# Performance work log

Measured on AMD Instinct MI355X. Metric: run time of the kernel, lower is better.

The kernel has to match this reference:

```python
import jax, jax.numpy as jnp
import numpy as np
from jax import lax

DN = ('NCHW', 'OIHW', 'NCHW')
EPS = 1e-5


def _conv3x3(x, w, b):
    return lax.conv_general_dilated(x, w, (1, 1), 'SAME', dimension_numbers=DN) + b[:, None, None]


def _conv1x1(x, w, b):
    return jnp.einsum('bchw,oc->bohw', x, w) + b[:, None, None]


def _dwconv3x3(x, w, b):
    # w: (C,1,3,3), depthwise
    C = x.shape[1]
    return lax.conv_general_dilated(x, w, (1, 1), 'SAME', feature_group_count=C,
                                    dimension_numbers=DN) + b[:, None, None]


def setup_inputs() -> dict:
    key = jax.random.key(0)
    ks = jax.random.split(key, 24)
    b, t, c, h, w = 2, 8, 64, 160, 160
    r, K = c // 4, 3

    def n(k, shape, s=0.05):
        return jax.random.normal(k, shape, dtype=jnp.float32) * s

    return {
        'feature': n(ks[0], (b, t, c, h, w), 1.0),
        'kc_w1': n(ks[1], (r, c)),
        'kc_bn_gamma': jnp.ones((r,), jnp.float32),
        'kc_bn_beta': jnp.zeros((r,), jnp.float32),
        'kc_bn_mean': jnp.zeros((r,), jnp.float32),
        'kc_bn_var': jnp.ones((r,), jnp.float32),
        'kc_w2': n(ks[2], (c * K * K, r)),
        'kc_b2': n(ks[3], (c * K * K,)),
        'kc_bias': n(ks[4], (c,)),
        'conv1_w': n(ks[5], (2 * c, 2 * c, 3, 3)),
        'conv1_b': n(ks[6], (2 * c,)),
        'pi1_w': n(ks[7], (4 * c, c)),
        'pi1_b': n(ks[8], (4 * c,)),
        'dw1_w': n(ks[9], (4 * c, 1, 3, 3)),
        'dw1_b': n(ks[10], (4 * c,)),
        'po1_w': n(ks[11], (c, 4 * c)),
        'po1_b': n(ks[12], (c,)),
        'pi2_w': n(ks[13], (4 * c, c)),
        'pi2_b': n(ks[14], (4 * c,)),
        'dw2_w': n(ks[15], (4 * c, 1, 3, 3)),
        'dw2_b': n(ks[16], (4 * c,)),
        'po2_w': n(ks[17], (c, 4 * c)),
        'po2_b': n(ks[18], (c,)),
    }


def reference(feature, kc_w1, kc_bn_gamma, kc_bn_beta, kc_bn_mean, kc_bn_var,
              kc_w2, kc_b2, kc_bias, conv1_w, conv1_b,
              pi1_w, pi1_b, dw1_w, dw1_b, po1_w, po1_b,
              pi2_w, pi2_b, dw2_w, dw2_b, po2_w, po2_b):
    b, t, c, h, w = feature.shape
    K = int(round((kc_w2.shape[0] // c) ** 0.5))  # dynamic kernel size (3)

    def dyn_dwconv(x_feat, y):
        # kernel generation: GAP -> 1x1 -> BN(eval) -> ReLU -> 1x1
        pool = x_feat.mean(axis=(2, 3))                           # (b, c)
        z = pool @ kc_w1.T                                        # (b, r)
        z = (z - kc_bn_mean) * jax.lax.rsqrt(kc_bn_var + EPS) * kc_bn_gamma + kc_bn_beta
        z = jax.nn.relu(z)
        wd = (z @ kc_w2.T + kc_b2).reshape(b, c, K, K)            # per-sample dw kernels

        def per_sample(yi, wi):
            return lax.conv_general_dilated(yi[None], wi[:, None], (1, 1), 'SAME',
                                            feature_group_count=c,
                                            dimension_numbers=DN)[0]
        out = jax.vmap(per_sample)(y, wd)                         # (b, c, h, w)
        return out + kc_bias[None, :, None, None]

    def step(feat_prop, x_feat):
        fp = dyn_dwconv(x_feat, feat_prop)
        fusion = jnp.concatenate([x_feat, fp], axis=1)
        fusion = jax.nn.leaky_relu(_conv3x3(fusion, conv1_w, conv1_b), 0.1)
        f1, f2 = fusion[:, :c], fusion[:, c:]
        g1 = jax.nn.sigmoid(_conv1x1(_dwconv3x3(_conv1x1(f1, pi1_w, pi1_b), dw1_w, dw1_b), po1_w, po1_b))
        g2 = jax.nn.sigmoid(_conv1x1(_dwconv3x3(_conv1x1(f2, pi2_w, pi2_b), dw2_w, dw2_b), po2_w, po2_b))
        new_fp = f1 * g1 + f2 * g2
        return new_fp, new_fp

    init = feature[:, t - 1]                                      # frame t-1
    xs = jnp.moveaxis(jnp.flip(feature[:, :t - 1], axis=1), 1, 0)  # frames t-2 .. 0
    _, ys = lax.scan(step, init, xs)                              # (t-1, b, c, h, w)
    full = jnp.concatenate([jnp.flip(ys, axis=0), init[None]], axis=0)
    return jnp.moveaxis(full, 0, 1)                               # (b, t, c, h, w)
```

## Files before the change

kernel.cpp:

```cpp
#include <hip/hip_runtime.h>

typedef __attribute__((ext_vector_type(8))) __bf16 bf16x8;
typedef __attribute__((ext_vector_type(4))) float f32x4;

#define BB 2
#define TT 8
#define CC 64
#define HH 160
#define WW 160
#define HWW 25600
#define RR 16
#define C2 128
#define C4 256
#define C8 512
#define NSTEP 7
#define CHW (CC*HWW)
#define EPSV 1e-5f

__device__ __forceinline__ f32x4 mfma16(bf16x8 a, bf16x8 b, f32x4 c) {
    return __builtin_amdgcn_mfma_f32_16x16x32_bf16(a, b, c, 0, 0, 0);
}

__global__ void pool_kernel(const float* __restrict__ feat, float* __restrict__ pool) {
    int idx = blockIdx.x;
    int b = idx / (NSTEP * CC);
    int f = (idx / CC) % NSTEP;
    int c = idx % CC;
    const float4* src = (const float4*)(feat + ((size_t)(b * TT + f) * CC + c) * HWW);
    float s = 0.f;
    for (int i = threadIdx.x; i < HWW / 4; i += 256) {
        float4 v = src[i];
        s += v.x + v.y + v.z + v.w;
    }
    __shared__ float sm[256];
    sm[threadIdx.x] = s;
    __syncthreads();
    for (int off = 128; off > 0; off >>= 1) {
        if (threadIdx.x < off) sm[threadIdx.x] += sm[threadIdx.x + off];
        __syncthreads();
    }
    if (threadIdx.x == 0) pool[idx] = sm[0] * (1.0f / HWW);
}

__global__ void wd_kernel(const float* __restrict__ pool, const float* __restrict__ w1,
                          const float* __restrict__ gamma, const float* __restrict__ beta,
                          const float* __restrict__ mean, const float* __restrict__ var,
                          const float* __restrict__ w2, const float* __restrict__ b2,
                          float* __restrict__ wdT) {
    int bf = blockIdx.x;
    __shared__ float z[RR];
    int tid = threadIdx.x;
    if (tid < RR) {
        const float* p = pool + bf * CC;
        float s = 0.f;
        for (int c = 0; c < CC; c++) s += p[c] * w1[tid * CC + c];
        s = (s - mean[tid]) * rsqrtf(var[tid] + EPSV) * gamma[tid] + beta[tid];
        z[tid] = s > 0.f ? s : 0.f;
    }
    __syncthreads();
    for (int o = tid; o < CC * 9; o += 64) {
        float s = b2[o];
        #pragma unroll
        for (int r = 0; r < RR; r++) s += z[r] * w2[o * RR + r];
        int c = o / 9, t = o % 9;
        wdT[bf * 576 + t * CC + c] = s;
    }
}

__global__ void copy_init_kernel(const float* __restrict__ feat, float* __restrict__ out) {
    int i = blockIdx.x * 256 + threadIdx.x;
    int n4 = CHW / 4;
    int b = i / n4;
    int r = i % n4;
    size_t off = ((size_t)(b * TT + (TT - 1)) * CHW) / 4 + r;
    ((float4*)out)[off] = ((const float4*)feat)[off];
}

__global__ void prep_weights(const float* __restrict__ c1w,
                             const float* __restrict__ pi1, const float* __restrict__ pi2,
                             const float* __restrict__ po1, const float* __restrict__ po2,
                             const float* __restrict__ dw1, const float* __restrict__ dw2,
                             const float* __restrict__ dw1b, const float* __restrict__ dw2b,
                             __bf16* __restrict__ Bc1,
                             __bf16* __restrict__ Bpi1, __bf16* __restrict__ Bpi2,
                             __bf16* __restrict__ Bpo1, __bf16* __restrict__ Bpo2,
                             float* __restrict__ dwT12, float* __restrict__ dwb12) {
    int idx = blockIdx.x * 256 + threadIdx.x;
    if (idx < 147456) {
        int oc = idx / 1152, k = idx % 1152;
        int t = k >> 7, ic = k & 127;
        Bc1[idx] = (__bf16)c1w[(oc * 128 + ic) * 9 + t];
        return;
    }
    idx -= 147456;
    if (idx < 16384) { Bpi1[idx] = (__bf16)pi1[idx]; return; }
    idx -= 16384;
    if (idx < 16384) { Bpi2[idx] = (__bf16)pi2[idx]; return; }
    idx -= 16384;
    if (idx < 16384) { Bpo1[idx] = (__bf16)po1[idx]; return; }
    idx -= 16384;
    if (idx < 16384) { Bpo2[idx] = (__bf16)po2[idx]; return; }
    idx -= 16384;
    if (idx < 4608) {
        int t = idx / 512, c = idx % 512;
        dwT12[t * C8 + c] = (c < 256) ? dw1[c * 9 + t] : dw2[(c - 256) * 9 + t];
        return;
    }
    idx -= 4608;
    if (idx < 512) { dwb12[idx] = (idx < 256) ? dw1b[idx] : dw2b[idx - 256]; }
}

__global__ void featPM_kernel(const float* __restrict__ feat, __bf16* __restrict__ featPM) {
    __shared__ float Lt[64 * 68];
    int bf = blockIdx.x / 400;
    int p0 = (blockIdx.x % 400) * 64;
    int tid = threadIdx.x;
    int c = tid & 63, half = tid >> 6;
    const float* src = feat + ((size_t)bf * CC + c) * HWW + p0 + half * 16;
    #pragma unroll
    for (int k = 0; k < 16; k++) Lt[(half * 16 + k) * 68 + c] = src[k];
    __syncthreads();
    int cg = tid & 7;
    #pragma unroll
    for (int pass = 0; pass < 2; pass++) {
        int pl = (tid >> 3) + pass * 32;
        bf16x8 o;
        #pragma unroll
        for (int j = 0; j < 8; j++) o[j] = (__bf16)Lt[pl * 68 + cg * 8 + j];
        *(bf16x8*)(featPM + ((size_t)bf * HWW + p0 + pl) * CC + cg * 8) = o;
    }
}

__global__ void dyndw_kernel(const __bf16* __restrict__ src, size_t bstr,
                             const float* __restrict__ wdT, const float* __restrict__ kc_bias,
                             __bf16* __restrict__ fpPM, int fx) {
    int gi = blockIdx.x * 256 + threadIdx.x;
    int c0 = (gi & 7) * 8;
    int rem = gi >> 3;
    int p = rem % HWW;
    int bb = rem / HWW;
    int py = p / WW, px = p % WW;
    float acc[8];
    float4 k0 = *(const float4*)(kc_bias + c0);
    float4 k1 = *(const float4*)(kc_bias + c0 + 4);
    acc[0]=k0.x; acc[1]=k0.y; acc[2]=k0.z; acc[3]=k0.w;
    acc[4]=k1.x; acc[5]=k1.y; acc[6]=k1.z; acc[7]=k1.w;
    const float* wb = wdT + (size_t)(bb * NSTEP + fx) * 576;
    const __bf16* sb = src + (size_t)bb * bstr;
    const int dyA[9] = {-1,-1,-1,0,0,0,1,1,1};
    const int dxA[9] = {-1,0,1,-1,0,1,-1,0,1};
    #pragma unroll
    for (int t = 0; t < 9; t++) {
        int dy = dyA[t], dx = dxA[t];
        if ((unsigned)(py + dy) < HH && (unsigned)(px + dx) < WW) {
            bf16x8 uv = *(const bf16x8*)(sb + (size_t)(p + dy * WW + dx) * CC + c0);
            float4 w0 = *(const float4*)(wb + t * CC + c0);
            float4 w1 = *(const float4*)(wb + t * CC + c0 + 4);
            acc[0] += (float)uv[0] * w0.x; acc[1] += (float)uv[1] * w0.y;
            acc[2] += (float)uv[2] * w0.z; acc[3] += (float)uv[3] * w0.w;
            acc[4] += (float)uv[4] * w1.x; acc[5] += (float)uv[5] * w1.y;
            acc[6] += (float)uv[6] * w1.z; acc[7] += (float)uv[7] * w1.w;
        }
    }
    bf16x8 o;
    #pragma unroll
    for (int j = 0; j < 8; j++) o[j] = (__bf16)acc[j];
    *(bf16x8*)(fpPM + ((size_t)bb * HWW + p) * CC + c0) = o;
}

__global__ void conv1_gemm(const __bf16* __restrict__ featPM, const __bf16* __restrict__ fpPM,
                           const __bf16* __restrict__ Bc1, const float* __restrict__ bias,
                           __bf16* __restrict__ fusionPM, int fx) {
    __shared__ __align__(16) __bf16 As[128 * 40];
    __shared__ __align__(16) __bf16 Bs[128 * 40];
    const int tid = threadIdx.x;
    const int bb = blockIdx.x / 200;
    const int p0 = (blockIdx.x % 200) * 128;
    const int i = tid >> 1, h = tid & 1;
    const int p = p0 + i;
    const int py = p / WW, px = p % WW;
    const __bf16* featB = featPM + (size_t)(bb * TT + fx) * HWW * CC;
    const __bf16* fpB   = fpPM + (size_t)bb * HWW * CC;
    const int wv = tid >> 6, lane = tid & 63, lm = lane & 15, lq = lane >> 4;
    f32x4 acc[2][8];
    #pragma unroll
    for (int mt = 0; mt < 2; mt++)
        #pragma unroll
        for (int nt = 0; nt < 8; nt++) acc[mt][nt] = (f32x4){0.f, 0.f, 0.f, 0.f};

    for (int ks = 0; ks < 36; ks++) {
        const int t = ks >> 2, ci0 = (ks & 3) * 32;
        const int dy = t / 3 - 1, dx = t % 3 - 1;
        const bool valid = ((unsigned)(py + dy) < HH) && ((unsigned)(px + dx) < WW);
        uint4 a0 = {0,0,0,0}, a1 = {0,0,0,0};
        if (valid) {
            const __bf16* sp = (ci0 < 64)
                ? featB + (size_t)(p + dy * WW + dx) * CC + ci0
                : fpB   + (size_t)(p + dy * WW + dx) * CC + (ci0 - 64);
            a0 = *(const uint4*)(sp + h * 16);
            a1 = *(const uint4*)(sp + h * 16 + 8);
        }
        const __bf16* bp = Bc1 + (size_t)i * 1152 + ks * 32 + h * 16;
        uint4 w0q = *(const uint4*)(bp);
        uint4 w1q = *(const uint4*)(bp + 8);
        __syncthreads();
        *(uint4*)&As[i * 40 + h * 16]     = a0;
        *(uint4*)&As[i * 40 + h * 16 + 8] = a1;
        *(uint4*)&Bs[i * 40 + h * 16]     = w0q;
        *(uint4*)&Bs[i * 40 + h * 16 + 8] = w1q;
        __syncthreads();
        bf16x8 af0 = *(const bf16x8*)&As[((wv * 2 + 0) * 16 + lm) * 40 + lq * 8];
        bf16x8 af1 = *(const bf16x8*)&As[((wv * 2 + 1) * 16 + lm) * 40 + lq * 8];
        #pragma unroll
        for (int nt = 0; nt < 8; nt++) {
            bf16x8 bf = *(const bf16x8*)&Bs[(nt * 16 + lm) * 40 + lq * 8];
            acc[0][nt] = mfma16(af0, bf, acc[0][nt]);
            acc[1][nt] = mfma16(af1, bf, acc[1][nt]);
        }
    }
    __bf16* ob = fusionPM + (size_t)bb * HWW * C2;
    #pragma unroll
    for (int mt = 0; mt < 2; mt++) {
        #pragma unroll
        for (int nt = 0; nt < 8; nt++) {
            const int oc = nt * 16 + lm;
            const float bs = bias[oc];
            #pragma unroll
            for (int r = 0; r < 4; r++) {
                const int pp = p0 + (wv * 2 + mt) * 16 + lq * 4 + r;
                float v = acc[mt][nt][r] + bs;
                v = v > 0.f ? v : 0.1f * v;
                ob[(size_t)pp * C2 + oc] = (__bf16)v;
            }
        }
    }
}

__global__ void pw1_gemm(const __bf16* __restrict__ fusionPM,
                         const __bf16* __restrict__ Bpi1, const __bf16* __restrict__ Bpi2,
                         const float* __restrict__ pi1b, const float* __restrict__ pi2b,
                         __bf16* __restrict__ u12PM) {
    __shared__ __align__(16) __bf16 As[128 * 40];
    __shared__ __align__(16) __bf16 Bs[128 * 40];
    const int tid = threadIdx.x;
    const int bb = blockIdx.x / 800;
    const int rem = blockIdx.x % 800;
    const int p0 = (rem >> 2) * 128;
    const int nb = rem & 3;
    const int br = nb >> 1, ns = nb & 1;
    const __bf16* Bpi = br ? Bpi2 : Bpi1;
    const float* bias = br ? pi2b : pi1b;
    const int i = tid >> 1, h = tid & 1;
    const int p = p0 + i;
    const __bf16* fB = fusionPM + (size_t)bb * HWW * C2 + br * CC;
    const int wv = tid >> 6, lane = tid & 63, lm = lane & 15, lq = lane >> 4;
    f32x4 acc[2][8];
    #pragma unroll
    for (int mt = 0; mt < 2; mt++)
        #pragma unroll
        for (int nt = 0; nt < 8; nt++) acc[mt][nt] = (f32x4){0.f, 0.f, 0.f, 0.f};

    #pragma unroll
    for (int ks = 0; ks < 2; ks++) {
        const int ci0 = ks * 32;
        const __bf16* sp = fB + (size_t)p * C2 + ci0 + h * 16;
        uint4 a0 = *(const uint4*)(sp);
        uint4 a1 = *(const uint4*)(sp + 8);
        const __bf16* bp = Bpi + (size_t)(ns * 128 + i) * 64 + ci0 + h * 16;
        uint4 w0q = *(const uint4*)(bp);
        uint4 w1q = *(const uint4*)(bp + 8);
        __syncthreads();
        *(uint4*)&As[i * 40 + h * 16]     = a0;
        *(uint4*)&As[i * 40 + h * 16 + 8] = a1;
        *(uint4*)&Bs[i * 40 + h * 16]     = w0q;
        *(uint4*)&Bs[i * 40 + h * 16 + 8] = w1q;
        __syncthreads();
        bf16x8 af0 = *(const bf16x8*)&As[((wv * 2 + 0) * 16 + lm) * 40 + lq * 8];
        bf16x8 af1 = *(const bf16x8*)&As[((wv * 2 + 1) * 16 + lm) * 40 + lq * 8];
        #pragma unroll
        for (int nt = 0; nt < 8; nt++) {
            bf16x8 bf = *(const bf16x8*)&Bs[(nt * 16 + lm) * 40 + lq * 8];
            acc[0][nt] = mfma16(af0, bf, acc[0][nt]);
            acc[1][nt] = mfma16(af1, bf, acc[1][nt]);
        }
    }
    __bf16* ub = u12PM + (size_t)bb * HWW * C8;
    #pragma unroll
    for (int mt = 0; mt < 2; mt++) {
        #pragma unroll
        for (int nt = 0; nt < 8; nt++) {
            const int ocl = ns * 128 + nt * 16 + lm;
            const int oc = br * 256 + ocl;
            const float bs = bias[ocl];
            #pragma unroll
            for (int r = 0; r < 4; r++) {
                const int pp = p0 + (wv * 2 + mt) * 16 + lq * 4 + r;
                ub[(size_t)pp * C8 + oc] = (__bf16)(acc[mt][nt][r] + bs);
            }
        }
    }
}

__global__ void dwv_kernel(const __bf16* __restrict__ u12PM, const float* __restrict__ dwT12,
                           const float* __restrict__ dwb12, __bf16* __restrict__ v12PM) {
    int gi = blockIdx.x * 256 + threadIdx.x;
    int c0 = (gi & 63) * 8;
    int rem = gi >> 6;
    int p = rem % HWW;
    int bb = rem / HWW;
    int py = p / WW, px = p % WW;
    float acc[8];
    float4 b0 = *(const float4*)(dwb12 + c0);
    float4 b1 = *(const float4*)(dwb12 + c0 + 4);
    acc[0]=b0.x; acc[1]=b0.y; acc[2]=b0.z; acc[3]=b0.w;
    acc[4]=b1.x; acc[5]=b1.y; acc[6]=b1.z; acc[7]=b1.w;
    const __bf16* ub = u12PM + (size_t)bb * HWW * C8;
    const int dyA[9] = {-1,-1,-1,0,0,0,1,1,1};
    const int dxA[9] = {-1,0,1,-1,0,1,-1,0,1};
    #pragma unroll
    for (int t = 0; t < 9; t++) {
        int dy = dyA[t], dx = dxA[t];
        if ((unsigned)(py + dy) < HH && (unsigned)(px + dx) < WW) {
            bf16x8 uv = *(const bf16x8*)(ub + (size_t)(p + dy * WW + dx) * C8 + c0);
            float4 w0 = *(const float4*)(dwT12 + t * C8 + c0);
            float4 w1 = *(const float4*)(dwT12 + t * C8 + c0 + 4);
            acc[0] += (float)uv[0] * w0.x; acc[1] += (float)uv[1] * w0.y;
            acc[2] += (float)uv[2] * w0.z; acc[3] += (float)uv[3] * w0.w;
            acc[4] += (float)uv[4] * w1.x; acc[5] += (float)uv[5] * w1.y;
            acc[6] += (float)uv[6] * w1.z; acc[7] += (float)uv[7] * w1.w;
        }
    }
    bf16x8 o;
    #pragma unroll
    for (int j = 0; j < 8; j++) o[j] = (__bf16)acc[j];
    *(bf16x8*)(v12PM + ((size_t)bb * HWW + p) * C8 + c0) = o;
}

__global__ void pw2_gemm(const __bf16* __restrict__ v12PM,
                         const __bf16* __restrict__ Bpo1, const __bf16* __restrict__ Bpo2,
                         const float* __restrict__ pob1, const float* __restrict__ pob2,
                         const __bf16* __restrict__ fusionPM,
                         float* __restrict__ out, __bf16* __restrict__ outPM, int fx) {
    __shared__ __align__(16) __bf16 As[128 * 40];
    __shared__ __align__(16) __bf16 Bs[64 * 40];
    const int tid = threadIdx.x;
    const int bb = blockIdx.x / 200;
    const int p0 = (blockIdx.x % 200) * 128;
    const int i = tid >> 1, h = tid & 1;
    const int p = p0 + i;
    const __bf16* vB = v12PM + (size_t)bb * HWW * C8;
    const int wv = tid >> 6, lane = tid & 63, lm = lane & 15, lq = lane >> 4;
    f32x4 acc[2][2][4];
    #pragma unroll
    for (int br = 0; br < 2; br++)
        #pragma unroll
        for (int mt = 0; mt < 2; mt++)
            #pragma unroll
            for (int nt = 0; nt < 4; nt++) acc[br][mt][nt] = (f32x4){0.f, 0.f, 0.f, 0.f};

    for (int ks = 0; ks < 16; ks++) {
        const int ci0 = ks * 32;
        const int br = ks >> 3;
        const __bf16* sp = vB + (size_t)p * C8 + ci0 + h * 16;
        uint4 a0 = *(const uint4*)(sp);
        uint4 a1 = *(const uint4*)(sp + 8);
        uint4 w0q = {0,0,0,0}, w1q = {0,0,0,0};
        if (tid < 128) {
            const __bf16* Bpo = br ? Bpo2 : Bpo1;
            const __bf16* bp = Bpo + (size_t)i * C4 + (ci0 & 255) + h * 16;
            w0q = *(const uint4*)(bp);
            w1q = *(const uint4*)(bp + 8);
        }
        __syncthreads();
        *(uint4*)&As[i * 40 + h * 16]     = a0;
        *(uint4*)&As[i * 40 + h * 16 + 8] = a1;
        if (tid < 128) {
            *(uint4*)&Bs[i * 40 + h * 16]     = w0q;
            *(uint4*)&Bs[i * 40 + h * 16 + 8] = w1q;
        }
        __syncthreads();
        bf16x8 af0 = *(const bf16x8*)&As[((wv * 2 + 0) * 16 + lm) * 40 + lq * 8];
        bf16x8 af1 = *(const bf16x8*)&As[((wv * 2 + 1) * 16 + lm) * 40 + lq * 8];
        #pragma unroll
        for (int nt = 0; nt < 4; nt++) {
            bf16x8 bf = *(const bf16x8*)&Bs[(nt * 16 + lm) * 40 + lq * 8];
            acc[br][0][nt] = mfma16(af0, bf, acc[br][0][nt]);
            acc[br][1][nt] = mfma16(af1, bf, acc[br][1][nt]);
        }
    }
    const __bf16* fB = fusionPM + (size_t)bb * HWW * C2;
    __bf16* opB = outPM + (size_t)bb * HWW * CC;
    #pragma unroll
    for (int mt = 0; mt < 2; mt++) {
        #pragma unroll
        for (int nt = 0; nt < 4; nt++) {
            const int oc = nt * 16 + lm;
            const float bs1 = pob1[oc];
            const float bs2 = pob2[oc];
            #pragma unroll
            for (int r = 0; r < 4; r++) {
                const int pp = p0 + (wv * 2 + mt) * 16 + lq * 4 + r;
                float g1 = 1.f / (1.f + __expf(-(acc[0][mt][nt][r] + bs1)));
                float g2 = 1.f / (1.f + __expf(-(acc[1][mt][nt][r] + bs2)));
                float f1 = (float)fB[(size_t)pp * C2 + oc];
                float f2 = (float)fB[(size_t)pp * C2 + CC + oc];
                float val = f1 * g1 + f2 * g2;
                out[((size_t)(bb * TT + fx) * CC + oc) * HWW + pp] = val;
                opB[(size_t)pp * CC + oc] = (__bf16)val;
            }
        }
    }
}

extern "C" void kernel_launch(void* const* d_in, const int* in_sizes, int n_in,
                              void* d_out, int out_size, void* d_ws, size_t ws_size,
                              hipStream_t stream) {
    const float* feat     = (const float*)d_in[0];
    const float* kc_w1    = (const float*)d_in[1];
    const float* kc_g     = (const float*)d_in[2];
    const float* kc_be    = (const float*)d_in[3];
    const float* kc_mu    = (const float*)d_in[4];
    const float* kc_var   = (const float*)d_in[5];
    const float* kc_w2    = (const float*)d_in[6];
    const float* kc_b2    = (const float*)d_in[7];
    const float* kc_bias  = (const float*)d_in[8];
    const float* conv1_w  = (const float*)d_in[9];
    const float* conv1_b  = (const float*)d_in[10];
    const float* pi1_w    = (const float*)d_in[11];
    const float* pi1_b    = (const float*)d_in[12];
    const float* dw1_w    = (const float*)d_in[13];
    const float* dw1_b    = (const float*)d_in[14];
    const float* po1_w    = (const float*)d_in[15];
    const float* po1_b    = (const float*)d_in[16];
    const float* pi2_w    = (const float*)d_in[17];
    const float* pi2_b    = (const float*)d_in[18];
    const float* dw2_w    = (const float*)d_in[19];
    const float* dw2_b    = (const float*)d_in[20];
    const float* po2_w    = (const float*)d_in[21];
    const float* po2_b    = (const float*)d_in[22];
    float* out = (float*)d_out;

    char* W = (char*)d_ws;
    __bf16* featPM   = (__bf16*)W; W += (size_t)BB * TT * HWW * CC * 2;
    __bf16* fpPM     = (__bf16*)W; W += (size_t)BB * HWW * CC * 2;
    __bf16* fusionPM = (__bf16*)W; W += (size_t)BB * HWW * C2 * 2;
    __bf16* u12PM    = (__bf16*)W; W += (size_t)BB * HWW * C8 * 2;
    __bf16* v12PM    = (__bf16*)W; W += (size_t)BB * HWW * C8 * 2;
    __bf16* outPM    = (__bf16*)W; W += (size_t)BB * HWW * CC * 2;
    __bf16* Bc1      = (__bf16*)W; W += 294912;
    __bf16* Bpi1     = (__bf16*)W; W += 32768;
    __bf16* Bpi2     = (__bf16*)W; W += 32768;
    __bf16* Bpo1     = (__bf16*)W; W += 32768;
    __bf16* Bpo2     = (__bf16*)W; W += 32768;
    float*  dwT12    = (float*)W;  W += 18432;
    float*  dwb12    = (float*)W;  W += 2048;
    float*  poolb    = (float*)W;  W += 4096;
    float*  wdT      = (float*)W;  W += 32256;

    prep_weights<<<852, 256, 0, stream>>>(conv1_w, pi1_w, pi2_w, po1_w, po2_w, dw1_w, dw2_w,
                                          dw1_b, dw2_b,
                                          Bc1, Bpi1, Bpi2, Bpo1, Bpo2, dwT12, dwb12);
    featPM_kernel<<<BB * TT * 400, 256, 0, stream>>>(feat, featPM);
    pool_kernel<<<BB * NSTEP * CC, 256, 0, stream>>>(feat, poolb);
    wd_kernel<<<BB * NSTEP, 64, 0, stream>>>(poolb, kc_w1, kc_g, kc_be, kc_mu, kc_var, kc_w2, kc_b2, wdT);
    copy_init_kernel<<<BB * CHW / 4 / 256, 256, 0, stream>>>(feat, out);

    for (int i = 0; i < NSTEP; i++) {
        int fx = NSTEP - 1 - i;
        const __bf16* src = (fx == NSTEP - 1) ? (featPM + (size_t)(TT - 1) * HWW * CC) : outPM;
        size_t bstr = (fx == NSTEP - 1) ? (size_t)TT * HWW * CC : (size_t)HWW * CC;
        dyndw_kernel<<<BB * HWW * 8 / 256, 256, 0, stream>>>(src, bstr, wdT, kc_bias, fpPM, fx);
        conv1_gemm<<<BB * 200, 256, 0, stream>>>(featPM, fpPM, Bc1, conv1_b, fusionPM, fx);
        pw1_gemm<<<BB * 800, 256, 0, stream>>>(fusionPM, Bpi1, Bpi2, pi1_b, pi2_b, u12PM);
        dwv_kernel<<<BB * HWW * 64 / 256, 256, 0, stream>>>(u12PM, dwT12, dwb12, v12PM);
        pw2_gemm<<<BB * 200, 256, 0, stream>>>(v12PM, Bpo1, Bpo2, po1_b, po2_b, fusionPM, out, outPM, fx);
    }
}
```

Baseline: 1.149 ms.

## Fuse depthwise 3x3 conv into pointwise-out GEMM via shared-memory staging

Merges the separate depthwise conv kernel into the second pointwise GEMM. Each block computes the depthwise output for its 128 pixels, one 128-channel chunk at a time, into LDS and feeds it straight to MFMA. The point is to drop the v12PM intermediate write and read-back plus one launch per step. The po weights are also pre-packed into an MFMA fragment layout and read directly from global memory, removing the B staging and syncs. The trade-off is that the depthwise work now runs on only 400 blocks, with wreg register pressure and lower occupancy, instead of a fully parallel elementwise kernel.

```diff
diff --git a/kernel.cpp b/kernel.cpp
--- a/kernel.cpp
+++ b/kernel.cpp
@@ -84,7 +84,8 @@
                              __bf16* __restrict__ Bc1,
                              __bf16* __restrict__ Bpi1, __bf16* __restrict__ Bpi2,
                              __bf16* __restrict__ Bpo1, __bf16* __restrict__ Bpo2,
-                             float* __restrict__ dwT12, float* __restrict__ dwb12) {
+                             float* __restrict__ dwT12, float* __restrict__ dwb12,
+                             __bf16* __restrict__ Bpk) {
     int idx = blockIdx.x * 256 + threadIdx.x;
     if (idx < 147456) {
         int oc = idx / 1152, k = idx % 1152;
@@ -107,7 +108,16 @@
         return;
     }
     idx -= 4608;
-    if (idx < 512) { dwb12[idx] = (idx < 256) ? dw1b[idx] : dw2b[idx - 256]; }
+    if (idx < 512) { dwb12[idx] = (idx < 256) ? dw1b[idx] : dw2b[idx - 256]; return; }
+    idx -= 512;
+    if (idx < 32768) {
+        int j = idx & 7, ln = (idx >> 3) & 63, nt = (idx >> 9) & 3, kg = (idx >> 11) & 3, cc = idx >> 13;
+        int lmx = ln & 15, lqx = ln >> 4;
+        int oc = nt * 16 + lmx;
+        int ci = (cc & 1) * 128 + kg * 32 + lqx * 8 + j;
+        const float* src = (cc >> 1) ? po2 : po1;
+        Bpk[idx] = (__bf16)src[oc * C4 + ci];
+    }
 }
 
 __global__ void featPM_kernel(const float* __restrict__ feat, __bf16* __restrict__ featPM) {
@@ -301,92 +311,88 @@
     }
 }
 
-__global__ void dwv_kernel(const __bf16* __restrict__ u12PM, const float* __restrict__ dwT12,
-                           const float* __restrict__ dwb12, __bf16* __restrict__ v12PM) {
-    int gi = blockIdx.x * 256 + threadIdx.x;
-    int c0 = (gi & 63) * 8;
-    int rem = gi >> 6;
-    int p = rem % HWW;
-    int bb = rem / HWW;
-    int py = p / WW, px = p % WW;
-    float acc[8];
-    float4 b0 = *(const float4*)(dwb12 + c0);
-    float4 b1 = *(const float4*)(dwb12 + c0 + 4);
-    acc[0]=b0.x; acc[1]=b0.y; acc[2]=b0.z; acc[3]=b0.w;
-    acc[4]=b1.x; acc[5]=b1.y; acc[6]=b1.z; acc[7]=b1.w;
-    const __bf16* ub = u12PM + (size_t)bb * HWW * C8;
-    const int dyA[9] = {-1,-1,-1,0,0,0,1,1,1};
-    const int dxA[9] = {-1,0,1,-1,0,1,-1,0,1};
-    #pragma unroll
-    for (int t = 0; t < 9; t++) {
-        int dy = dyA[t], dx = dxA[t];
-        if ((unsigned)(py + dy) < HH && (unsigned)(px + dx) < WW) {
-            bf16x8 uv = *(const bf16x8*)(ub + (size_t)(p + dy * WW + dx) * C8 + c0);
-            float4 w0 = *(const float4*)(dwT12 + t * C8 + c0);
-            float4 w1 = *(const float4*)(dwT12 + t * C8 + c0 + 4);
-            acc[0] += (float)uv[0] * w0.x; acc[1] += (float)uv[1] * w0.y;
-            acc[2] += (float)uv[2] * w0.z; acc[3] += (float)uv[3] * w0.w;
-            acc[4] += (float)uv[4] * w1.x; acc[5] += (float)uv[5] * w1.y;
-            acc[6] += (float)uv[6] * w1.z; acc[7] += (float)uv[7] * w1.w;
-        }
-    }
-    bf16x8 o;
-    #pragma unroll
-    for (int j = 0; j < 8; j++) o[j] = (__bf16)acc[j];
-    *(bf16x8*)(v12PM + ((size_t)bb * HWW + p) * C8 + c0) = o;
-}
-
-__global__ void pw2_gemm(const __bf16* __restrict__ v12PM,
-                         const __bf16* __restrict__ Bpo1, const __bf16* __restrict__ Bpo2,
-                         const float* __restrict__ pob1, const float* __restrict__ pob2,
-                         const __bf16* __restrict__ fusionPM,
-                         float* __restrict__ out, __bf16* __restrict__ outPM, int fx) {
-    __shared__ __align__(16) __bf16 As[128 * 40];
-    __shared__ __align__(16) __bf16 Bs[64 * 40];
+__global__ void dwpw2_gemm(const __bf16* __restrict__ u12PM,
+                           const float* __restrict__ dwT12, const float* __restrict__ dwb12,
+                           const __bf16* __restrict__ Bpk,
+                           const float* __restrict__ pob1, const float* __restrict__ pob2,
+                           const __bf16* __restrict__ fusionPM,
+                           float* __restrict__ out, __bf16* __restrict__ outPM, int fx) {
+    __shared__ __align__(16) __bf16 Vt[128 * 136];
     const int tid = threadIdx.x;
     const int bb = blockIdx.x / 200;
     const int p0 = (blockIdx.x % 200) * 128;
-    const int i = tid >> 1, h = tid & 1;
-    const int p = p0 + i;
-    const __bf16* vB = v12PM + (size_t)bb * HWW * C8;
+    const __bf16* uB = u12PM + (size_t)bb * HWW * C8;
     const int wv = tid >> 6, lane = tid & 63, lm = lane & 15, lq = lane >> 4;
-    f32x4 acc[2][2][4];
-    #pragma unroll
-    for (int br = 0; br < 2; br++)
-        #pragma unroll
-        for (int mt = 0; mt < 2; mt++)
-            #pragma unroll
-            for (int nt = 0; nt < 4; nt++) acc[br][mt][nt] = (f32x4){0.f, 0.f, 0.f, 0.f};
-
-    for (int ks = 0; ks < 16; ks++) {
-        const int ci0 = ks * 32;
-        const int br = ks >> 3;
-        const __bf16* sp = vB + (size_t)p * C8 + ci0 + h * 16;
-        uint4 a0 = *(const uint4*)(sp);
-        uint4 a1 = *(const uint4*)(sp + 8);
-        uint4 w0q = {0,0,0,0}, w1q = {0,0,0,0};
-        if (tid < 128) {
-            const __bf16* Bpo = br ? Bpo2 : Bpo1;
-            const __bf16* bp = Bpo + (size_t)i * C4 + (ci0 & 255) + h * 16;
-            w0q = *(const uint4*)(bp);
-            w1q = *(const uint4*)(bp + 8);
-        }
-        __syncthreads();
-        *(uint4*)&As[i * 40 + h * 16]     = a0;
-        *(uint4*)&As[i * 40 + h * 16 + 8] = a1;
-        if (tid < 128) {
-            *(uint4*)&Bs[i * 40 + h * 16]     = w0q;
-            *(uint4*)&Bs[i * 40 + h * 16 + 8] = w1q;
-        }
-        __syncthreads();
-        bf16x8 af0 = *(const bf16x8*)&As[((wv * 2 + 0) * 16 + lm) * 40 + lq * 8];
-        bf16x8 af1 = *(const bf16x8*)&As[((wv * 2 + 1) * 16 + lm) * 40 + lq * 8];
+    const int cg = tid & 15, cl = cg * 8, prow = tid >> 4;
+    f32x4 accA[2][4], accB[2][4];
+    #pragma unroll
+    for (int mt = 0; mt < 2; mt++)
         #pragma unroll
         for (int nt = 0; nt < 4; nt++) {
-            bf16x8 bf = *(const bf16x8*)&Bs[(nt * 16 + lm) * 40 + lq * 8];
-            acc[br][0][nt] = mfma16(af0, bf, acc[br][0][nt]);
-            acc[br][1][nt] = mfma16(af1, bf, acc[br][1][nt]);
-        }
+            accA[mt][nt] = (f32x4){0.f, 0.f, 0.f, 0.f};
+            accB[mt][nt] = (f32x4){0.f, 0.f, 0.f, 0.f};
+        }
+
+    for (int cc = 0; cc < 4; cc++) {
+        float wreg[9][8];
+        #pragma unroll
+        for (int t = 0; t < 9; t++) {
+            float4 w0 = *(const float4*)(dwT12 + t * C8 + cc * 128 + cl);
+            float4 w1 = *(const float4*)(dwT12 + t * C8 + cc * 128 + cl + 4);
+            wreg[t][0] = w0.x; wreg[t][1] = w0.y; wreg[t][2] = w0.z; wreg[t][3] = w0.w;
+            wreg[t][4] = w1.x; wreg[t][5] = w1.y; wreg[t][6] = w1.z; wreg[t][7] = w1.w;
+        }
+        float4 b0 = *(const float4*)(dwb12 + cc * 128 + cl);
+        float4 b1 = *(const float4*)(dwb12 + cc * 128 + cl + 4);
+        const int dyA[9] = {-1,-1,-1,0,0,0,1,1,1};
+        const int dxA[9] = {-1,0,1,-1,0,1,-1,0,1};
+        for (int it = 0; it < 8; it++) {
+            const int pl = it * 16 + prow;
+            const int p = p0 + pl;
+            const int py = p / WW, px = p % WW;
+            float accv[8] = {b0.x, b0.y, b0.z, b0.w, b1.x, b1.y, b1.z, b1.w};
+            #pragma unroll
+            for (int t = 0; t < 9; t++) {
+                const int dy = dyA[t], dx = dxA[t];
+                if ((unsigned)(py + dy) < HH && (unsigned)(px + dx) < WW) {
+                    bf16x8 uv = *(const bf16x8*)(uB + (size_t)(p + dy * WW + dx) * C8 + cc * 128 + cl);
+                    #pragma unroll
+                    for (int j = 0; j < 8; j++) accv[j] += (float)uv[j] * wreg[t][j];
+                }
+            }
+            bf16x8 o;
+            #pragma unroll
+            for (int j = 0; j < 8; j++) o[j] = (__bf16)accv[j];
+            *(bf16x8*)&Vt[pl * 136 + cl] = o;
+        }
+        __syncthreads();
+        const __bf16* bbase = Bpk + cc * 8192 + (size_t)lane * 8;
+        if (cc < 2) {
+            #pragma unroll
+            for (int kg = 0; kg < 4; kg++) {
+                bf16x8 af0 = *(const bf16x8*)&Vt[((wv * 2 + 0) * 16 + lm) * 136 + kg * 32 + lq * 8];
+                bf16x8 af1 = *(const bf16x8*)&Vt[((wv * 2 + 1) * 16 + lm) * 136 + kg * 32 + lq * 8];
+                #pragma unroll
+                for (int nt = 0; nt < 4; nt++) {
+                    bf16x8 bfr = *(const bf16x8*)(bbase + kg * 2048 + nt * 512);
+                    accA[0][nt] = mfma16(af0, bfr, accA[0][nt]);
+                    accA[1][nt] = mfma16(af1, bfr, accA[1][nt]);
+                }
+            }
+        } else {
+            #pragma unroll
+            for (int kg = 0; kg < 4; kg++) {
+                bf16x8 af0 = *(const bf16x8*)&Vt[((wv * 2 + 0) * 16 + lm) * 136 + kg * 32 + lq * 8];
+                bf16x8 af1 = *(const bf16x8*)&Vt[((wv * 2 + 1) * 16 + lm) * 136 + kg * 32 + lq * 8];
+                #pragma unroll
+                for (int nt = 0; nt < 4; nt++) {
+                    bf16x8 bfr = *(const bf16x8*)(bbase + kg * 2048 + nt * 512);
+                    accB[0][nt] = mfma16(af0, bfr, accB[0][nt]);
+                    accB[1][nt] = mfma16(af1, bfr, accB[1][nt]);
+                }
+            }
+        }
+        __syncthreads();
     }
     const __bf16* fB = fusionPM + (size_t)bb * HWW * C2;
     __bf16* opB = outPM + (size_t)bb * HWW * CC;
@@ -400,8 +406,8 @@
             #pragma unroll
             for (int r = 0; r < 4; r++) {
                 const int pp = p0 + (wv * 2 + mt) * 16 + lq * 4 + r;
-                float g1 = 1.f / (1.f + __expf(-(acc[0][mt][nt][r] + bs1)));
-                float g2 = 1.f / (1.f + __expf(-(acc[1][mt][nt][r] + bs2)));
+                float g1 = 1.f / (1.f + __expf(-(accA[mt][nt][r] + bs1)));
+                float g2 = 1.f / (1.f + __expf(-(accB[mt][nt][r] + bs2)));
                 float f1 = (float)fB[(size_t)pp * C2 + oc];
                 float f2 = (float)fB[(size_t)pp * C2 + CC + oc];
                 float val = f1 * g1 + f2 * g2;
@@ -445,21 +451,21 @@
     __bf16* fpPM     = (__bf16*)W; W += (size_t)BB * HWW * CC * 2;
     __bf16* fusionPM = (__bf16*)W; W += (size_t)BB * HWW * C2 * 2;
     __bf16* u12PM    = (__bf16*)W; W += (size_t)BB * HWW * C8 * 2;
-    __bf16* v12PM    = (__bf16*)W; W += (size_t)BB * HWW * C8 * 2;
     __bf16* outPM    = (__bf16*)W; W += (size_t)BB * HWW * CC * 2;
     __bf16* Bc1      = (__bf16*)W; W += 294912;
     __bf16* Bpi1     = (__bf16*)W; W += 32768;
     __bf16* Bpi2     = (__bf16*)W; W += 32768;
     __bf16* Bpo1     = (__bf16*)W; W += 32768;
     __bf16* Bpo2     = (__bf16*)W; W += 32768;
+    __bf16* Bpk      = (__bf16*)W; W += 65536;
     float*  dwT12    = (float*)W;  W += 18432;
     float*  dwb12    = (float*)W;  W += 2048;
     float*  poolb    = (float*)W;  W += 4096;
     float*  wdT      = (float*)W;  W += 32256;
 
-    prep_weights<<<852, 256, 0, stream>>>(conv1_w, pi1_w, pi2_w, po1_w, po2_w, dw1_w, dw2_w,
+    prep_weights<<<980, 256, 0, stream>>>(conv1_w, pi1_w, pi2_w, po1_w, po2_w, dw1_w, dw2_w,
                                           dw1_b, dw2_b,
-                                          Bc1, Bpi1, Bpi2, Bpo1, Bpo2, dwT12, dwb12);
+                                          Bc1, Bpi1, Bpi2, Bpo1, Bpo2, dwT12, dwb12, Bpk);
     featPM_kernel<<<BB * TT * 400, 256, 0, stream>>>(feat, featPM);
     pool_kernel<<<BB * NSTEP * CC, 256, 0, stream>>>(feat, poolb);
     wd_kernel<<<BB * NSTEP, 64, 0, stream>>>(poolb, kc_w1, kc_g, kc_be, kc_mu, kc_var, kc_w2, kc_b2, wdT);
@@ -472,7 +478,6 @@
         dyndw_kernel<<<BB * HWW * 8 / 256, 256, 0, stream>>>(src, bstr, wdT, kc_bias, fpPM, fx);
         conv1_gemm<<<BB * 200, 256, 0, stream>>>(featPM, fpPM, Bc1, conv1_b, fusionPM, fx);
         pw1_gemm<<<BB * 800, 256, 0, stream>>>(fusionPM, Bpi1, Bpi2, pi1_b, pi2_b, u12PM);
-        dwv_kernel<<<BB * HWW * 64 / 256, 256, 0, stream>>>(u12PM, dwT12, dwb12, v12PM);
-        pw2_gemm<<<BB * 200, 256, 0, stream>>>(v12PM, Bpo1, Bpo2, po1_b, po2_b, fusionPM, out, outPM, fx);
-    }
-}
+        dwpw2_gemm<<<BB * 200, 256, 0, stream>>>(u12PM, dwT12, dwb12, Bpk, po1_b, po2_b, fusionPM, out, outPM, fx);
+    }
+}
```

After: 1.623 ms. +41.2%, slower.
